# Kernel tuning notes

Measured on AMD Instinct MI355X. Metric: run time of the kernel, lower is better.

## Reference

```python
import jax, jax.numpy as jnp
import numpy as np

B, TD, TE, V, D, DFF, L, H = 16, 256, 1024, 5000, 512, 2048, 6, 8

def setup_inputs():
    key = jax.random.key(0)
    ks = jax.random.split(key, 32)
    s = 0.02
    def w(k, shape):
        return jax.random.normal(k, shape, jnp.float32) * s
    # targets drawn in [3, V) so the eos filter in the torch code is a no-op
    inp = {
        "targets": jax.random.randint(ks[0], (B, TD), 3, V),
        "target_lengths": jax.random.randint(ks[1], (B,), TD // 2, TD + 1),
        "encoder_outputs": jax.random.normal(ks[2], (B, TE, D), jnp.float32),
        "encoder_output_lengths": jax.random.randint(ks[3], (B,), TE // 2, TE + 1),
        "emb": w(ks[4], (V, D)),
        "W_in": w(ks[5], (D, D)), "b_in": jnp.zeros((D,), jnp.float32),
        "ln1_g": jnp.ones((L, D), jnp.float32), "ln1_b": jnp.zeros((L, D), jnp.float32),
        "Wq1": w(ks[6], (L, D, D)), "bq1": jnp.zeros((L, D), jnp.float32),
        "Wk1": w(ks[7], (L, D, D)), "bk1": jnp.zeros((L, D), jnp.float32),
        "Wv1": w(ks[8], (L, D, D)), "bv1": jnp.zeros((L, D), jnp.float32),
        "Wo1": w(ks[9], (L, D, D)), "bo1": jnp.zeros((L, D), jnp.float32),
        "ln2_g": jnp.ones((L, D), jnp.float32), "ln2_b": jnp.zeros((L, D), jnp.float32),
        "Wq2": w(ks[10], (L, D, D)), "bq2": jnp.zeros((L, D), jnp.float32),
        "Wk2": w(ks[11], (L, D, D)), "bk2": jnp.zeros((L, D), jnp.float32),
        "Wv2": w(ks[12], (L, D, D)), "bv2": jnp.zeros((L, D), jnp.float32),
        "Wo2": w(ks[13], (L, D, D)), "bo2": jnp.zeros((L, D), jnp.float32),
        "ln3_g": jnp.ones((L, D), jnp.float32), "ln3_b": jnp.zeros((L, D), jnp.float32),
        "W_ff1": w(ks[14], (L, D, DFF)), "b_ff1": jnp.zeros((L, DFF), jnp.float32),
        "W_ff2": w(ks[15], (L, DFF, D)), "b_ff2": jnp.zeros((L, D), jnp.float32),
    }
    return inp

def _ln(x, g, b, eps=1e-5):
    m = x.mean(-1, keepdims=True)
    v = ((x - m) ** 2).mean(-1, keepdims=True)
    return (x - m) * jax.lax.rsqrt(v + eps) * g + b

def _mha(q, k, v, Wq, bq, Wk, bk, Wv, bv, Wo, bo, mask):
    Bq, Tq, Dm = q.shape
    dh = Dm // H
    def heads(x, W, bias):
        y = x @ W + bias
        return y.reshape(x.shape[0], x.shape[1], H, dh).transpose(0, 2, 1, 3)  # (B,H,T,dh)
    qh, kh, vh = heads(q, Wq, bq), heads(k, Wk, bk), heads(v, Wv, bv)
    sc = jnp.einsum('bhqd,bhkd->bhqk', qh, kh) / jnp.sqrt(jnp.float32(dh))
    sc = jnp.where(mask[:, None, :, :], jnp.float32(-1e9), sc)
    a = jax.nn.softmax(sc, axis=-1)
    ctx = jnp.einsum('bhqk,bhkd->bhqd', a, vh).transpose(0, 2, 1, 3).reshape(Bq, Tq, Dm)
    return ctx @ Wo + bo

def _pos_encoding(length, dim):
    pos = jnp.arange(length, dtype=jnp.float32)[:, None]
    div = jnp.exp(jnp.arange(0, dim, 2, dtype=jnp.float32) * (-jnp.log(jnp.float32(10000.0)) / dim))
    pe = jnp.zeros((length, dim), jnp.float32)
    pe = pe.at[:, 0::2].set(jnp.sin(pos * div)).at[:, 1::2].set(jnp.cos(pos * div))
    return pe

def _forward(targets, target_lengths, encoder_output_lengths, encoder_outputs, emb, W_in, b_in, ln1_g, ln1_b, Wq1, bq1, Wk1, bk1, Wv1, bv1, Wo1, bo1, ln2_g, ln2_b, Wq2, bq2, Wk2, bk2, Wv2, bv2, Wo2, bo2, ln3_g, ln3_b, W_ff1, b_ff1, W_ff2, b_ff2):
    Bsz, Td = targets.shape
    Te = encoder_outputs.shape[1]
    key_pad = jnp.arange(Td)[None, :] >= target_lengths[:, None]            # (B, Td) pad keys
    causal = jnp.triu(jnp.ones((Td, Td), bool), k=1)                        # subsequent mask
    self_mask = key_pad[:, None, :] | causal[None]                          # (B, Td, Td)
    enc_pad = jnp.arange(Te)[None, :] >= encoder_output_lengths[:, None]    # (B, Te)
    enc_mask = jnp.broadcast_to(enc_pad[:, None, :], (Bsz, Td, Te))
    # TransformerEmbedding: lookup * sqrt(dim), then sinusoidal PE, then input_proj
    x = emb[targets] * jnp.sqrt(jnp.float32(D)) + _pos_encoding(Td, D)[None]
    x = x @ W_in + b_in
    for l in range(L):  # pre-LN decoder layers: self-attn, cross-attn, FFN
        h = _ln(x, ln1_g[l], ln1_b[l])
        x = x + _mha(h, h, h, Wq1[l], bq1[l], Wk1[l], bk1[l], Wv1[l], bv1[l], Wo1[l], bo1[l], self_mask)
        h = _ln(x, ln2_g[l], ln2_b[l])
        x = x + _mha(h, encoder_outputs, encoder_outputs, Wq2[l], bq2[l], Wk2[l], bk2[l], Wv2[l], bv2[l], Wo2[l], bo2[l], enc_mask)
        h = _ln(x, ln3_g[l], ln3_b[l])
        x = x + (jax.nn.relu(h @ W_ff1[l] + b_ff1[l]) @ W_ff2[l] + b_ff2[l])
    # torch code stacks step_outputs[:, di, :] over di, i.e. returns the hidden states (B, Td, D)
    return x

def reference(targets, target_lengths, encoder_outputs, encoder_output_lengths, emb, W_in, b_in, ln1_g, ln1_b, Wq1, bq1, Wk1, bk1, Wv1, bv1, Wo1, bo1, ln2_g, ln2_b, Wq2, bq2, Wk2, bk2, Wv2, bv2, Wo2, bo2, ln3_g, ln3_b, W_ff1, b_ff1, W_ff2, b_ff2):
    return _forward(targets, target_lengths, encoder_output_lengths, encoder_outputs, emb, W_in, b_in, ln1_g, ln1_b, Wq1, bq1, Wk1, bk1, Wv1, bv1, Wo1, bo1, ln2_g, ln2_b, Wq2, bq2, Wk2, bk2, Wv2, bv2, Wo2, bo2, ln3_g, ln3_b, W_ff1, b_ff1, W_ff2, b_ff2)
```

## Files before the change

kernel.cpp:

```cpp
#include <hip/hip_runtime.h>
#include <hip/hip_bf16.h>

#define BB   16
#define TD   256
#define TE   1024
#define DM   512
#define DFF  2048
#define NL   6
#define NH   8
#define DH   64

typedef unsigned short u16;
typedef unsigned int u32;
typedef short short8 __attribute__((ext_vector_type(8)));
typedef float f32x4 __attribute__((ext_vector_type(4)));

__device__ __forceinline__ float b2f(u16 u) {
    unsigned int x = ((unsigned int)u) << 16;
    float f;
    __builtin_memcpy(&f, &x, 4);
    return f;
}
__device__ __forceinline__ u16 f2b(float f) {
    unsigned int x;
    __builtin_memcpy(&x, &f, 4);
    unsigned int r = x + 0x7fffu + ((x >> 16) & 1u);
    return (u16)(r >> 16);
}

__device__ __forceinline__ void gload_lds16(const u16* g, u16* l) {
    __builtin_amdgcn_global_load_lds(
        (const __attribute__((address_space(1))) unsigned int*)g,
        (__attribute__((address_space(3))) unsigned int*)l, 16, 0, 0);
}

__global__ __launch_bounds__(256) void cvt_kernel(const float* __restrict__ in,
                                                  u16* __restrict__ out, int n4) {
    int i = blockIdx.x * 256 + threadIdx.x;
    if (i < n4) {
        float4 v = reinterpret_cast<const float4*>(in)[i];
        ushort4 o;
        o.x = f2b(v.x); o.y = f2b(v.y); o.z = f2b(v.z); o.w = f2b(v.w);
        reinterpret_cast<ushort4*>(out)[i] = o;
    }
}

template <int NMAT>
struct PtrArr { const float* p[NMAT]; };

template <int NMAT>
__global__ __launch_bounds__(256) void tr_kernel(PtrArr<NMAT> P, u16* __restrict__ out,
                                                 int K, int N) {
    __shared__ u16 t[64][65];
    const float* W = P.p[blockIdx.z];
    u16* O = out + (size_t)blockIdx.z * K * N;
    int n0 = blockIdx.x * 64, k0 = blockIdx.y * 64;
    int tid = threadIdx.x;
    int r = tid >> 4, c = (tid & 15) * 4;
#pragma unroll
    for (int p = 0; p < 4; ++p) {
        int k = r + p * 16;
        float4 v = *reinterpret_cast<const float4*>(&W[(size_t)(k0 + k) * N + n0 + c]);
        t[c + 0][k] = f2b(v.x);
        t[c + 1][k] = f2b(v.y);
        t[c + 2][k] = f2b(v.z);
        t[c + 3][k] = f2b(v.w);
    }
    __syncthreads();
#pragma unroll
    for (int p = 0; p < 4; ++p) {
        int n = r + p * 16;
        ushort4 o;
        o.x = t[n][c]; o.y = t[n][c + 1]; o.z = t[n][c + 2]; o.w = t[n][c + 3];
        *reinterpret_cast<ushort4*>(&O[(size_t)(n0 + n) * K + k0 + c]) = o;
    }
}

__global__ __launch_bounds__(256) void embed_kernel(const int* __restrict__ targets,
                                                    const float* __restrict__ emb,
                                                    u16* __restrict__ out) {
    int row = blockIdx.x;
    int t   = row & (TD - 1);
    int tgt = targets[row];
    const float c = -0.017988946039015984f;
    for (int d = threadIdx.x; d < DM; d += 256) {
        float e   = emb[(size_t)tgt * DM + d] * 22.627416997969522f;
        int   i2  = d & ~1;
        float div = expf(c * (float)i2);
        float arg = (float)t * div;
        float pe  = (d & 1) ? cosf(arg) : sinf(arg);
        out[(size_t)row * DM + d] = f2b(e + pe);
    }
}

__global__ __launch_bounds__(256) void ln_kernel(const float* __restrict__ X,
                                                 const float* __restrict__ g,
                                                 const float* __restrict__ b,
                                                 size_t vo,
                                                 u16* __restrict__ O) {
    int row = blockIdx.x;
    const float* xr = X + (size_t)row * DM;
    int tid = threadIdx.x;
    float v0 = xr[tid], v1 = xr[tid + 256];
    float s = v0 + v1;
    __shared__ float red[4];
    int lane = tid & 63, wid = tid >> 6;
#pragma unroll
    for (int off = 32; off; off >>= 1) s += __shfl_xor(s, off);
    if (lane == 0) red[wid] = s;
    __syncthreads();
    float mean = (red[0] + red[1] + red[2] + red[3]) * (1.0f / 512.0f);
    float d0 = v0 - mean, d1 = v1 - mean;
    float sq = d0 * d0 + d1 * d1;
#pragma unroll
    for (int off = 32; off; off >>= 1) sq += __shfl_xor(sq, off);
    __syncthreads();
    if (lane == 0) red[wid] = sq;
    __syncthreads();
    float var = (red[0] + red[1] + red[2] + red[3]) * (1.0f / 512.0f);
    float rs  = rsqrtf(var + 1e-5f);
    O[(size_t)row * DM + tid]       = f2b(d0 * rs * g[vo + tid]       + b[vo + tid]);
    O[(size_t)row * DM + tid + 256] = f2b(d1 * rs * g[vo + tid + 256] + b[vo + tid + 256]);
}

template <int TM, int TN, bool OUTBF, bool RELU, bool RES>
__global__ __launch_bounds__(256) void gemm_bt(const u16* __restrict__ A,
                                               const u16* __restrict__ Bt,
                                               const float* __restrict__ bias, size_t bofs,
                                               const float* __restrict__ resid,
                                               void* __restrict__ C,
                                               int M, int N, int K) {
    __shared__ u16 As[2][TM * 32];
    __shared__ u16 Bs[2][TN * 32];
    int tid = threadIdx.x, wave = tid >> 6, lane = tid & 63;
    int col0 = blockIdx.x * TN, row0 = blockIdx.y * TM;
    constexpr int WM = TM / 2, WN = TN / 2;
    int wm = (wave >> 1) * WM, wn = (wave & 1) * WN;
    int lq = lane >> 4, lc = lane & 15;
    constexpr int NI = WM / 16, NJ = WN / 16;
    f32x4 acc[NI][NJ] = {};
    int srow = lane >> 2;
    int scol = (lane & 3) * 8;

    auto stage = [&](int buf, int k0) {
#pragma unroll
        for (int s = 0; s < TM / 64; ++s) {
            int rbase = wave * (TM / 4) + s * 16;
            gload_lds16(A + (size_t)(row0 + rbase + srow) * K + k0 + scol, &As[buf][rbase * 32]);
        }
#pragma unroll
        for (int s = 0; s < TN / 64; ++s) {
            int rbase = wave * (TN / 4) + s * 16;
            gload_lds16(Bt + (size_t)(col0 + rbase + srow) * K + k0 + scol, &Bs[buf][rbase * 32]);
        }
    };

    stage(0, 0);
    __syncthreads();
    int cur = 0;
    for (int k0 = 0; k0 < K; k0 += 32) {
        if (k0 + 32 < K) stage(cur ^ 1, k0 + 32);
        short8 af[NI], bf[NJ];
#pragma unroll
        for (int i = 0; i < NI; ++i)
            af[i] = *reinterpret_cast<const short8*>(&As[cur][(wm + i * 16 + lc) * 32 + lq * 8]);
#pragma unroll
        for (int j = 0; j < NJ; ++j)
            bf[j] = *reinterpret_cast<const short8*>(&Bs[cur][(wn + j * 16 + lc) * 32 + lq * 8]);
#pragma unroll
        for (int i = 0; i < NI; ++i)
#pragma unroll
            for (int j = 0; j < NJ; ++j)
                acc[i][j] = __builtin_amdgcn_mfma_f32_16x16x32_bf16(af[i], bf[j], acc[i][j], 0, 0, 0);
        __syncthreads();
        cur ^= 1;
    }

#pragma unroll
    for (int j = 0; j < NJ; ++j) {
        int n = col0 + wn + j * 16 + lc;
        float bv = bias[bofs + n];
#pragma unroll
        for (int i = 0; i < NI; ++i) {
#pragma unroll
            for (int r = 0; r < 4; ++r) {
                int m = row0 + wm + i * 16 + lq * 4 + r;
                float v = acc[i][j][r] + bv;
                if (RES)  v += resid[(size_t)m * N + n];
                if (RELU) v = fmaxf(v, 0.0f);
                if (OUTBF) ((u16*)C)[(size_t)m * N + n] = f2b(v);
                else       ((float*)C)[(size_t)m * N + n] = v;
            }
        }
    }
}

template <int NG>
struct MOut { u16* out[NG]; const float* bias[NG]; };

template <int TM, int TN, int NG>
__global__ __launch_bounds__(256) void gemm_bt_multi(const u16* __restrict__ A,
                                                     const u16* __restrict__ Bt,
                                                     MOut<NG> mo, int K,
                                                     const int* __restrict__ lens,
                                                     int rbShift) {
    __shared__ u16 As[2][TM * 32];
    __shared__ u16 Bs[2][TN * 32];
    int tid = threadIdx.x, wave = tid >> 6, lane = tid & 63;
    int col0 = blockIdx.x * TN, row0 = blockIdx.y * TM;

    if (lens) {
        int bb  = row0 >> rbShift;
        int rl  = row0 & ((1 << rbShift) - 1);
        int lim = (lens[bb] + 63) & ~63;
        if (rl >= lim) return;
    }

    constexpr int WM = TM / 2, WN = TN / 2;
    int wm = (wave >> 1) * WM, wn = (wave & 1) * WN;
    int lq = lane >> 4, lc = lane & 15;
    constexpr int NI = WM / 16, NJ = WN / 16;
    f32x4 acc[NI][NJ] = {};
    int srow = lane >> 2;
    int scol = (lane & 3) * 8;

    auto stage = [&](int buf, int k0) {
#pragma unroll
        for (int s = 0; s < TM / 64; ++s) {
            int rbase = wave * (TM / 4) + s * 16;
            gload_lds16(A + (size_t)(row0 + rbase + srow) * K + k0 + scol, &As[buf][rbase * 32]);
        }
#pragma unroll
        for (int s = 0; s < TN / 64; ++s) {
            int rbase = wave * (TN / 4) + s * 16;
            gload_lds16(Bt + (size_t)(col0 + rbase + srow) * K + k0 + scol, &Bs[buf][rbase * 32]);
        }
    };

    stage(0, 0);
    __syncthreads();
    int cur = 0;
    for (int k0 = 0; k0 < K; k0 += 32) {
        if (k0 + 32 < K) stage(cur ^ 1, k0 + 32);
        short8 af[NI], bf[NJ];
#pragma unroll
        for (int i = 0; i < NI; ++i)
            af[i] = *reinterpret_cast<const short8*>(&As[cur][(wm + i * 16 + lc) * 32 + lq * 8]);
#pragma unroll
        for (int j = 0; j < NJ; ++j)
            bf[j] = *reinterpret_cast<const short8*>(&Bs[cur][(wn + j * 16 + lc) * 32 + lq * 8]);
#pragma unroll
        for (int i = 0; i < NI; ++i)
#pragma unroll
            for (int j = 0; j < NJ; ++j)
                acc[i][j] = __builtin_amdgcn_mfma_f32_16x16x32_bf16(af[i], bf[j], acc[i][j], 0, 0, 0);
        __syncthreads();
        cur ^= 1;
    }

    int g  = col0 >> 9;
    int c0 = col0 & 511;
    u16* O = mo.out[g];
    const float* bp = mo.bias[g];
#pragma unroll
    for (int j = 0; j < NJ; ++j) {
        int n = c0 + wn + j * 16 + lc;
        float bv = bp[n];
#pragma unroll
        for (int i = 0; i < NI; ++i) {
#pragma unroll
            for (int r = 0; r < 4; ++r) {
                int m = row0 + wm + i * 16 + lq * 4 + r;
                O[(size_t)m * 512 + n] = f2b(acc[i][j][r] + bv);
            }
        }
    }
}

#define QSTR 72

__device__ __forceinline__ int vidx(int d, int kp) {
    return d * 32 + (kp ^ (((d >> 2) & 7) << 2));
}

__global__ __launch_bounds__(256) void fattn_mfma(const u16* __restrict__ Q,
                                                  const u16* __restrict__ K,
                                                  const u16* __restrict__ V,
                                                  const int* __restrict__ lens,
                                                  u16* __restrict__ O,
                                                  int Tq, int Tk, int causal) {
    __shared__ u16 Qs[64 * QSTR];
    __shared__ u16 Ks[64 * QSTR];
    __shared__ u16 Ps[64 * QSTR];
    __shared__ u32 Vs32[64 * 32];
    int tid  = threadIdx.x;
    int qt0  = blockIdx.x * 64;
    int h    = blockIdx.y;
    int b    = blockIdx.z;
    int len  = lens[b];
    int wave = tid >> 6, lane = tid & 63;
    int lq = lane >> 4, lc = lane & 15;
    int sr = tid >> 4;
    int sd = (tid & 15) * 4;

    short8 bones;
    {
        u16 v = (lc == 0) ? (u16)0x3F80 : (u16)0;
        u16 tmp[8] = { v, v, v, v, v, v, v, v };
        __builtin_memcpy(&bones, tmp, 16);
    }

#pragma unroll
    for (int i = 0; i < 4; ++i) {
        int q = sr + i * 16;
        ushort4 v = *reinterpret_cast<const ushort4*>(
            &Q[(size_t)(b * Tq + qt0 + q) * DM + h * DH + sd]);
        ushort4 w;
        w.x = f2b(b2f(v.x) * 0.125f); w.y = f2b(b2f(v.y) * 0.125f);
        w.z = f2b(b2f(v.z) * 0.125f); w.w = f2b(b2f(v.w) * 0.125f);
        *reinterpret_cast<ushort4*>(&Qs[q * QSTR + sd]) = w;
    }

    ushort4 kr[4], vr[2][2];
#pragma unroll
    for (int i = 0; i < 4; ++i) {
        int k = sr + i * 16;
        kr[i] = *reinterpret_cast<const ushort4*>(&K[(size_t)(b * Tk + k) * DM + h * DH + sd]);
    }
#pragma unroll
    for (int i = 0; i < 2; ++i) {
        int kp = sr + i * 16;
#pragma unroll
        for (int p = 0; p < 2; ++p)
            vr[i][p] = *reinterpret_cast<const ushort4*>(
                &V[(size_t)(b * Tk + 2 * kp + p) * DM + h * DH + sd]);
    }
#pragma unroll
    for (int i = 0; i < 4; ++i) {
        int k = sr + i * 16;
        *reinterpret_cast<ushort4*>(&Ks[k * QSTR + sd]) = kr[i];
    }
#pragma unroll
    for (int i = 0; i < 2; ++i) {
        int kp = sr + i * 16;
        u16 a0[4], a1[4];
        __builtin_memcpy(a0, &vr[i][0], 8);
        __builtin_memcpy(a1, &vr[i][1], 8);
#pragma unroll
        for (int j = 0; j < 4; ++j)
            Vs32[vidx(sd + j, kp)] = (u32)a0[j] | ((u32)a1[j] << 16);
    }
    __syncthreads();

    short8 aq0 = *reinterpret_cast<const short8*>(&Qs[(wave * 16 + lc) * QSTR + lq * 8]);
    short8 aq1 = *reinterpret_cast<const short8*>(&Qs[(wave * 16 + lc) * QSTR + 32 + lq * 8]);

    f32x4 Ow[4] = {};
    f32x4 Ol = {};

    int kend = causal ? min(len, qt0 + 64) : len;
    for (int kt0 = 0; kt0 < kend; kt0 += 64) {
        bool more = (kt0 + 64) < kend;
        if (more) {
#pragma unroll
            for (int i = 0; i < 4; ++i) {
                int k = kt0 + 64 + sr + i * 16;
                kr[i] = *reinterpret_cast<const ushort4*>(
                    &K[(size_t)(b * Tk + k) * DM + h * DH + sd]);
            }
#pragma unroll
            for (int i = 0; i < 2; ++i) {
                int kp = sr + i * 16;
#pragma unroll
                for (int p = 0; p < 2; ++p)
                    vr[i][p] = *reinterpret_cast<const ushort4*>(
                        &V[(size_t)(b * Tk + kt0 + 64 + 2 * kp + p) * DM + h * DH + sd]);
            }
        }

        f32x4 sa[4] = {};
#pragma unroll
        for (int n = 0; n < 4; ++n) {
            short8 bk0 = *reinterpret_cast<const short8*>(&Ks[(n * 16 + lc) * QSTR + lq * 8]);
            short8 bk1 = *reinterpret_cast<const short8*>(&Ks[(n * 16 + lc) * QSTR + 32 + lq * 8]);
            sa[n] = __builtin_amdgcn_mfma_f32_16x16x32_bf16(aq0, bk0, sa[n], 0, 0, 0);
            sa[n] = __builtin_amdgcn_mfma_f32_16x16x32_bf16(aq1, bk1, sa[n], 0, 0, 0);
        }

        int qrow_base = qt0 + wave * 16 + lq * 4;
#pragma unroll
        for (int r = 0; r < 4; ++r) {
            int qrow = qrow_base + r;
#pragma unroll
            for (int n = 0; n < 4; ++n) {
                int key = kt0 + n * 16 + lc;
                bool inv = (key >= len) || (causal && key > qrow);
                float p = inv ? 0.0f : __expf(sa[n][r] - 8.0f);
                Ps[(wave * 16 + lq * 4 + r) * QSTR + n * 16 + lc] = f2b(p);
            }
        }

        short8 ap0 = *reinterpret_cast<const short8*>(&Ps[(wave * 16 + lc) * QSTR + lq * 8]);
        short8 ap1 = *reinterpret_cast<const short8*>(&Ps[(wave * 16 + lc) * QSTR + 32 + lq * 8]);
#pragma unroll
        for (int n = 0; n < 4; ++n) {
            int d = n * 16 + lc;
#pragma unroll
            for (int ks = 0; ks < 2; ++ks) {
                int base = d * 32 + ((ks * 16 + lq * 4) ^ (((d >> 2) & 7) << 2));
                uint4 vv = *reinterpret_cast<const uint4*>(&Vs32[base]);
                short8 bv;
                __builtin_memcpy(&bv, &vv, 16);
                Ow[n] = __builtin_amdgcn_mfma_f32_16x16x32_bf16(ks ? ap1 : ap0, bv, Ow[n], 0, 0, 0);
            }
        }
        Ol = __builtin_amdgcn_mfma_f32_16x16x32_bf16(ap0, bones, Ol, 0, 0, 0);
        Ol = __builtin_amdgcn_mfma_f32_16x16x32_bf16(ap1, bones, Ol, 0, 0, 0);

        __syncthreads();
        if (more) {
#pragma unroll
            for (int i = 0; i < 4; ++i) {
                int k = sr + i * 16;
                *reinterpret_cast<ushort4*>(&Ks[k * QSTR + sd]) = kr[i];
            }
#pragma unroll
            for (int i = 0; i < 2; ++i) {
                int kp = sr + i * 16;
                u16 a0[4], a1[4];
                __builtin_memcpy(a0, &vr[i][0], 8);
                __builtin_memcpy(a1, &vr[i][1], 8);
#pragma unroll
                for (int j = 0; j < 4; ++j)
                    Vs32[vidx(sd + j, kp)] = (u32)a0[j] | ((u32)a1[j] << 16);
            }
            __syncthreads();
        }
    }

#pragma unroll
    for (int r = 0; r < 4; ++r) {
        float lsum = __shfl(Ol[r], lane & 48);
        float inv = 1.0f / lsum;
        size_t rowoff = (size_t)(b * Tq + qt0 + wave * 16 + lq * 4 + r) * DM + h * DH;
#pragma unroll
        for (int n = 0; n < 4; ++n)
            O[rowoff + n * 16 + lc] = f2b(Ow[n][r] * inv);
    }
}

__global__ __launch_bounds__(256) void store_out_kernel(const float* __restrict__ X,
                                                        float* __restrict__ out, int n) {
    int i = blockIdx.x * 256 + threadIdx.x;
    if (i < n) out[i] = X[i];
}

extern "C" void kernel_launch(void* const* d_in, const int* in_sizes, int n_in,
                              void* d_out, int out_size, void* d_ws, size_t ws_size,
                              hipStream_t stream) {
    const int*   targets = (const int*)d_in[0];
    const int*   tlen    = (const int*)d_in[1];
    const float* enc     = (const float*)d_in[2];
    const int*   elen    = (const int*)d_in[3];
    const float* emb     = (const float*)d_in[4];
    const float* W_in    = (const float*)d_in[5];
    const float* b_in    = (const float*)d_in[6];
    const float* ln1_g   = (const float*)d_in[7];
    const float* ln1_b   = (const float*)d_in[8];
    const float* Wq1 = (const float*)d_in[9],  *bq1 = (const float*)d_in[10];
    const float* Wk1 = (const float*)d_in[11], *bk1 = (const float*)d_in[12];
    const float* Wv1 = (const float*)d_in[13], *bv1 = (const float*)d_in[14];
    const float* Wo1 = (const float*)d_in[15], *bo1 = (const float*)d_in[16];
    const float* ln2_g = (const float*)d_in[17], *ln2_b = (const float*)d_in[18];
    const float* Wq2 = (const float*)d_in[19], *bq2 = (const float*)d_in[20];
    const float* Wk2 = (const float*)d_in[21], *bk2 = (const float*)d_in[22];
    const float* Wv2 = (const float*)d_in[23], *bv2 = (const float*)d_in[24];
    const float* Wo2 = (const float*)d_in[25], *bo2 = (const float*)d_in[26];
    const float* ln3_g = (const float*)d_in[27], *ln3_b = (const float*)d_in[28];
    const float* W_ff1 = (const float*)d_in[29], *b_ff1 = (const float*)d_in[30];
    const float* W_ff2 = (const float*)d_in[31], *b_ff2 = (const float*)d_in[32];

    float* ws   = (float*)d_ws;
    float* x    = ws;
    u16*   hb   = (u16*)(ws + 2097152);
    u16*   qb   = (u16*)(ws + 3145728);
    u16*   ctx  = (u16*)(ws + 4194304);
    u16*   kb   = (u16*)(ws + 5242880);
    u16*   vb   = (u16*)(ws + 9437184);
    u16*   encb = (u16*)(ws + 13631488);
    u16*   wt_dm = (u16*)(ws + 17825792);
    u16*   wt_f1 = (u16*)(ws + 24248320);
    u16*   wt_f2 = (u16*)(ws + 27394048);
    u16*   ffh  = kb;

    PtrArr<49> pdm;
    pdm.p[0] = W_in;
    for (int l = 0; l < NL; ++l) {
        const float* ws8[8] = { Wq1, Wk1, Wv1, Wo1, Wq2, Wk2, Wv2, Wo2 };
        for (int j = 0; j < 8; ++j) pdm.p[1 + l * 8 + j] = ws8[j] + (size_t)l * DM * DM;
    }
    PtrArr<6> pf1, pf2;
    for (int l = 0; l < NL; ++l) {
        pf1.p[l] = W_ff1 + (size_t)l * DM * DFF;
        pf2.p[l] = W_ff2 + (size_t)l * DFF * DM;
    }
    tr_kernel<49><<<dim3(8, 8, 49), 256, 0, stream>>>(pdm, wt_dm, 512, 512);
    tr_kernel<6><<<dim3(32, 8, 6), 256, 0, stream>>>(pf1, wt_f1, 512, 2048);
    tr_kernel<6><<<dim3(8, 32, 6), 256, 0, stream>>>(pf2, wt_f2, 2048, 512);

    const size_t WDM = (size_t)512 * 512;
    const size_t WFF = (size_t)512 * 2048;

    const dim3 gdm(8, 64);
    const dim3 gqkv(24, 64);
    const dim3 gkv2(8, 128);
    const dim3 gf1(16, 32);
    const dim3 gattn(TD / 64, NH, BB);

    cvt_kernel<<<8192, 256, 0, stream>>>(enc, encb, BB * TE * DM / 4);
    embed_kernel<<<4096, 256, 0, stream>>>(targets, emb, hb);
    gemm_bt<64, 64, false, false, false><<<gdm, 256, 0, stream>>>(hb, wt_dm, b_in, 0, nullptr, x, 4096, 512, 512);

    for (int l = 0; l < NL; ++l) {
        const size_t vo = (size_t)l * DM;
        const size_t fv = (size_t)l * DFF;
        const u16* tq1 = wt_dm + (1 + l * 8 + 0) * WDM;
        const u16* to1 = wt_dm + (1 + l * 8 + 3) * WDM;
        const u16* tq2 = wt_dm + (1 + l * 8 + 4) * WDM;
        const u16* tk2 = wt_dm + (1 + l * 8 + 5) * WDM;
        const u16* to2 = wt_dm + (1 + l * 8 + 7) * WDM;
        const u16* tf1 = wt_f1 + l * WFF;
        const u16* tf2 = wt_f2 + l * WFF;

        ln_kernel<<<4096, 256, 0, stream>>>(x, ln1_g, ln1_b, vo, hb);
        {
            MOut<3> mo;
            mo.out[0] = qb; mo.out[1] = kb; mo.out[2] = vb;
            mo.bias[0] = bq1 + vo; mo.bias[1] = bk1 + vo; mo.bias[2] = bv1 + vo;
            gemm_bt_multi<64, 64, 3><<<gqkv, 256, 0, stream>>>(hb, tq1, mo, 512, nullptr, 0);
        }
        fattn_mfma<<<gattn, 256, 0, stream>>>(qb, kb, vb, tlen, ctx, TD, TD, 1);
        gemm_bt<64, 64, false, false, true><<<gdm, 256, 0, stream>>>(ctx, to1, bo1, vo, x, x, 4096, 512, 512);

        ln_kernel<<<4096, 256, 0, stream>>>(x, ln2_g, ln2_b, vo, hb);
        gemm_bt<64, 64, true, false, false><<<gdm, 256, 0, stream>>>(hb, tq2, bq2, vo, nullptr, qb, 4096, 512, 512);
        {
            MOut<2> mo;
            mo.out[0] = kb; mo.out[1] = vb;
            mo.bias[0] = bk2 + vo; mo.bias[1] = bv2 + vo;
            gemm_bt_multi<128, 128, 2><<<gkv2, 256, 0, stream>>>(encb, tk2, mo, 512, elen, 10);
        }
        fattn_mfma<<<gattn, 256, 0, stream>>>(qb, kb, vb, elen, ctx, TD, TE, 0);
        gemm_bt<64, 64, false, false, true><<<gdm, 256, 0, stream>>>(ctx, to2, bo2, vo, x, x, 4096, 512, 512);

        ln_kernel<<<4096, 256, 0, stream>>>(x, ln3_g, ln3_b, vo, hb);
        gemm_bt<128, 128, true, true, false><<<gf1, 256, 0, stream>>>(hb, tf1, b_ff1, fv, nullptr, ffh, 4096, 2048, 512);
        gemm_bt<64, 64, false, false, true><<<gdm, 256, 0, stream>>>(ffh, tf2, b_ff2, vo, x, x, 4096, 512, 2048);
    }

    store_out_kernel<<<8192, 256, 0, stream>>>(x, (float*)d_out, BB * TD * DM);
}
```

Measured before the change: 1.341 ms.

## Group cross-attn Q with K/V GEMM, skip padded rows, fast unmasked softmax path

Generalizes the multi-output GEMM so each output group has its own A matrix, row limit and length-skip flag. The cross-attention Q projection now runs in the same launch as the encoder K/V projections, removing one kernel launch per layer. Self-attention K/V row tiles past the padded target length are skipped. The attention kernel gains a fast path that leaves out per-element masking when a key tile is fully valid. This adds idle blocks in the grouped grid (Q rows stop at 4096) and uses 128x128 tiles for the Q GEMM, which may balance work less evenly.

```diff
diff --git a/kernel.cpp b/kernel.cpp
--- a/kernel.cpp
+++ b/kernel.cpp
@@ -196,25 +196,35 @@
 }
 
 template <int NG>
-struct MOut { u16* out[NG]; const float* bias[NG]; };
+struct MGrp {
+    const u16* A[NG];
+    u16* out[NG];
+    const float* bias[NG];
+    int mlim[NG];
+    int skip[NG];
+};
 
 template <int TM, int TN, int NG>
-__global__ __launch_bounds__(256) void gemm_bt_multi(const u16* __restrict__ A,
+__global__ __launch_bounds__(256) void gemm_bt_multi(MGrp<NG> mg,
                                                      const u16* __restrict__ Bt,
-                                                     MOut<NG> mo, int K,
+                                                     int K,
                                                      const int* __restrict__ lens,
                                                      int rbShift) {
     __shared__ u16 As[2][TM * 32];
     __shared__ u16 Bs[2][TN * 32];
     int tid = threadIdx.x, wave = tid >> 6, lane = tid & 63;
     int col0 = blockIdx.x * TN, row0 = blockIdx.y * TM;
-
-    if (lens) {
+    int g  = col0 >> 9;
+    int c0 = col0 & 511;
+
+    if (row0 >= mg.mlim[g]) return;
+    if (mg.skip[g]) {
         int bb  = row0 >> rbShift;
         int rl  = row0 & ((1 << rbShift) - 1);
         int lim = (lens[bb] + 63) & ~63;
         if (rl >= lim) return;
     }
+    const u16* A = mg.A[g];
 
     constexpr int WM = TM / 2, WN = TN / 2;
     int wm = (wave >> 1) * WM, wn = (wave & 1) * WN;
@@ -258,10 +268,8 @@
         cur ^= 1;
     }
 
-    int g  = col0 >> 9;
-    int c0 = col0 & 511;
-    u16* O = mo.out[g];
-    const float* bp = mo.bias[g];
+    u16* O = mg.out[g];
+    const float* bp = mg.bias[g];
 #pragma unroll
     for (int j = 0; j < NJ; ++j) {
         int n = c0 + wn + j * 16 + lc;
@@ -388,15 +396,26 @@
         }
 
         int qrow_base = qt0 + wave * 16 + lq * 4;
-#pragma unroll
-        for (int r = 0; r < 4; ++r) {
-            int qrow = qrow_base + r;
-#pragma unroll
-            for (int n = 0; n < 4; ++n) {
-                int key = kt0 + n * 16 + lc;
-                bool inv = (key >= len) || (causal && key > qrow);
-                float p = inv ? 0.0f : __expf(sa[n][r] - 8.0f);
-                Ps[(wave * 16 + lq * 4 + r) * QSTR + n * 16 + lc] = f2b(p);
+        bool nomask = (kt0 + 64 <= len) &&
+                      (!causal || (kt0 + 63 <= qt0 + wave * 16));
+        if (nomask) {
+#pragma unroll
+            for (int r = 0; r < 4; ++r)
+#pragma unroll
+                for (int n = 0; n < 4; ++n)
+                    Ps[(wave * 16 + lq * 4 + r) * QSTR + n * 16 + lc] =
+                        f2b(__expf(sa[n][r] - 8.0f));
+        } else {
+#pragma unroll
+            for (int r = 0; r < 4; ++r) {
+                int qrow = qrow_base + r;
+#pragma unroll
+                for (int n = 0; n < 4; ++n) {
+                    int key = kt0 + n * 16 + lc;
+                    bool inv = (key >= len) || (causal && key > qrow);
+                    float p = inv ? 0.0f : __expf(sa[n][r] - 8.0f);
+                    Ps[(wave * 16 + lq * 4 + r) * QSTR + n * 16 + lc] = f2b(p);
+                }
             }
         }
 
@@ -513,7 +532,7 @@
 
     const dim3 gdm(8, 64);
     const dim3 gqkv(24, 64);
-    const dim3 gkv2(8, 128);
+    const dim3 gq2kv(12, 128);
     const dim3 gf1(16, 32);
     const dim3 gattn(TD / 64, NH, BB);
 
@@ -527,28 +546,32 @@
         const u16* tq1 = wt_dm + (1 + l * 8 + 0) * WDM;
         const u16* to1 = wt_dm + (1 + l * 8 + 3) * WDM;
         const u16* tq2 = wt_dm + (1 + l * 8 + 4) * WDM;
-        const u16* tk2 = wt_dm + (1 + l * 8 + 5) * WDM;
         const u16* to2 = wt_dm + (1 + l * 8 + 7) * WDM;
         const u16* tf1 = wt_f1 + l * WFF;
         const u16* tf2 = wt_f2 + l * WFF;
 
         ln_kernel<<<4096, 256, 0, stream>>>(x, ln1_g, ln1_b, vo, hb);
         {
-            MOut<3> mo;
-            mo.out[0] = qb; mo.out[1] = kb; mo.out[2] = vb;
-            mo.bias[0] = bq1 + vo; mo.bias[1] = bk1 + vo; mo.bias[2] = bv1 + vo;
-            gemm_bt_multi<64, 64, 3><<<gqkv, 256, 0, stream>>>(hb, tq1, mo, 512, nullptr, 0);
+            MGrp<3> mg;
+            mg.A[0] = hb;  mg.A[1] = hb;  mg.A[2] = hb;
+            mg.out[0] = qb; mg.out[1] = kb; mg.out[2] = vb;
+            mg.bias[0] = bq1 + vo; mg.bias[1] = bk1 + vo; mg.bias[2] = bv1 + vo;
+            mg.mlim[0] = 4096; mg.mlim[1] = 4096; mg.mlim[2] = 4096;
+            mg.skip[0] = 0; mg.skip[1] = 1; mg.skip[2] = 1;
+            gemm_bt_multi<64, 64, 3><<<gqkv, 256, 0, stream>>>(mg, tq1, 512, tlen, 8);
         }
         fattn_mfma<<<gattn, 256, 0, stream>>>(qb, kb, vb, tlen, ctx, TD, TD, 1);
         gemm_bt<64, 64, false, false, true><<<gdm, 256, 0, stream>>>(ctx, to1, bo1, vo, x, x, 4096, 512, 512);
 
         ln_kernel<<<4096, 256, 0, stream>>>(x, ln2_g, ln2_b, vo, hb);
-        gemm_bt<64, 64, true, false, false><<<gdm, 256, 0, stream>>>(hb, tq2, bq2, vo, nullptr, qb, 4096, 512, 512);
         {
-            MOut<2> mo;
-            mo.out[0] = kb; mo.out[1] = vb;
-            mo.bias[0] = bk2 + vo; mo.bias[1] = bv2 + vo;
-            gemm_bt_multi<128, 128, 2><<<gkv2, 256, 0, stream>>>(encb, tk2, mo, 512, elen, 10);
+            MGrp<3> mg;
+            mg.A[0] = hb;  mg.A[1] = encb; mg.A[2] = encb;
+            mg.out[0] = qb; mg.out[1] = kb; mg.out[2] = vb;
+            mg.bias[0] = bq2 + vo; mg.bias[1] = bk2 + vo; mg.bias[2] = bv2 + vo;
+            mg.mlim[0] = 4096; mg.mlim[1] = 16384; mg.mlim[2] = 16384;
+            mg.skip[0] = 0; mg.skip[1] = 1; mg.skip[2] = 1;
+            gemm_bt_multi<128, 128, 3><<<gq2kv, 256, 0, stream>>>(mg, tq2, 512, elen, 10);
         }
         fattn_mfma<<<gattn, 256, 0, stream>>>(qb, kb, vb, elen, ctx, TD, TE, 0);
         gemm_bt<64, 64, false, false, true><<<gdm, 256, 0, stream>>>(ctx, to2, bo2, vo, x, x, 4096, 512, 512);
```

After: 1.291 ms. -3.7%, faster.
